# Kernel optimization log

Measured on AMD Instinct MI355X. Metric: run time of the kernel, lower is better.

Reference implementation:

```python
import jax, jax.numpy as jnp
import numpy as np

VOCAB = 32000
HID = 256
B = 16
S = 256


def setup_inputs() -> dict:
    key = jax.random.key(0)
    ks = jax.random.split(key, 8)
    old = jax.random.randint(ks[0], (B, S), 0, VOCAB)
    emb = jax.random.normal(ks[1], (VOCAB, HID), dtype=jnp.float32) * 0.05
    # PyTorch LSTM packs gates as [i, f, g, o] along dim 0 of weight matrices
    W_ih = jax.random.normal(ks[2], (4 * HID, HID), dtype=jnp.float32) * 0.05
    W_hh = jax.random.normal(ks[3], (4 * HID, HID), dtype=jnp.float32) * 0.05
    b_ih = jax.random.normal(ks[4], (4 * HID,), dtype=jnp.float32) * 0.05
    b_hh = jax.random.normal(ks[5], (4 * HID,), dtype=jnp.float32) * 0.05
    W_lin = jax.random.normal(ks[6], (VOCAB, HID), dtype=jnp.float32) * 0.05
    b_lin = jax.random.normal(ks[7], (VOCAB,), dtype=jnp.float32) * 0.05
    return {"old": old, "emb": emb, "W_ih": W_ih, "W_hh": W_hh,
            "b_ih": b_ih, "b_hh": b_hh, "W_lin": W_lin, "b_lin": b_lin}


def reference(old, emb, W_ih, W_hh, b_ih, b_hh, W_lin, b_lin):
    # Teacher forcing (teacher_ratio=0.5 is truthy in the original, so the
    # input at step l is always old[:, l-1]). ret[:, l] = logits after
    # consuming old[:, l-1]; final return is ret[:, 1:] -> [B, S-1, V].
    emb_eff = emb.at[0].set(0.0)          # padding_idx=0
    tokens = old[:, : S - 1]               # [B, T] with T = S-1
    x = emb_eff[tokens]                    # [B, T, H]
    x_t = jnp.swapaxes(x, 0, 1)            # [T, B, H] time-major for scan

    def step(carry, xt):
        h, c = carry
        gates = xt @ W_ih.T + b_ih + h @ W_hh.T + b_hh   # [B, 4H]
        i, f, g, o = jnp.split(gates, 4, axis=-1)
        c = jax.nn.sigmoid(f) * c + jax.nn.sigmoid(i) * jnp.tanh(g)
        h = jax.nn.sigmoid(o) * jnp.tanh(c)
        return (h, c), h

    h0 = jnp.zeros((B, HID), dtype=x.dtype)
    c0 = jnp.zeros((B, HID), dtype=x.dtype)
    _, hs = jax.lax.scan(step, (h0, c0), x_t)            # [T, B, H]
    logits = hs @ W_lin.T + b_lin                        # [T, B, V]
    return jnp.swapaxes(logits, 0, 1)                    # [B, T, V]
```

## Files before the change

### kernel.cpp

```cpp
#include <hip/hip_runtime.h>
#include <hip/hip_bf16.h>
#include <stdint.h>
#include <stddef.h>

#define VOCAB 32000
#define HID 256
#define BATCH 16
#define SEQ 256
#define TSTEPS 255
#define NGATES 1024
#define NWG 4
#define MROWS (TSTEPS*BATCH)

typedef __attribute__((ext_vector_type(8))) __bf16 bf16x8;
typedef __attribute__((ext_vector_type(8))) short short8;
typedef __attribute__((ext_vector_type(4))) float floatx4;

__device__ __forceinline__ float sigmoidf_(float x) {
    return 1.0f / (1.0f + __expf(-x));
}
__device__ __forceinline__ float tanhf_(float x) {
    return 2.0f / (1.0f + __expf(-2.0f * x)) - 1.0f;
}

__device__ __forceinline__ bf16x8 cvt8(const float* __restrict__ p) {
    const floatx4* q = (const floatx4*)p;
    floatx4 x = q[0], y = q[1];
    bf16x8 r;
    r[0] = (__bf16)x[0]; r[1] = (__bf16)x[1]; r[2] = (__bf16)x[2]; r[3] = (__bf16)x[3];
    r[4] = (__bf16)y[0]; r[5] = (__bf16)y[1]; r[6] = (__bf16)y[2]; r[7] = (__bf16)y[3];
    return r;
}

__global__ __launch_bounds__(256) void k_cvt(const float* __restrict__ src,
                                             __bf16* __restrict__ dst) {
    size_t i = ((size_t)blockIdx.x * 256 + threadIdx.x) * 8;
    bf16x8 r = cvt8(src + i);
    *(bf16x8*)(dst + i) = r;
}

__global__ __launch_bounds__(256) void k_xw(const int* __restrict__ old,
                                            const float* __restrict__ emb,
                                            const __bf16* __restrict__ wih,
                                            const float* __restrict__ b_ih,
                                            const float* __restrict__ b_hh,
                                            float* __restrict__ xw) {
    int t = blockIdx.x;
    int tid = threadIdx.x;
    int wave = tid >> 6, lane = tid & 63, quad = lane >> 4, l16 = lane & 15;

    int tok = old[l16 * SEQ + t];
    bf16x8 a[8];
#pragma unroll
    for (int kt = 0; kt < 8; kt++) {
        if (tok == 0) {
            bf16x8 z;
#pragma unroll
            for (int j = 0; j < 8; j++) z[j] = (__bf16)0.0f;
            a[kt] = z;
        } else {
            a[kt] = cvt8(emb + (size_t)tok * HID + kt * 32 + quad * 8);
        }
    }

    float* xwt = xw + (size_t)t * NGATES * BATCH;
    for (int nt = 0; nt < 16; nt++) {
        int n = wave * 256 + nt * 16 + l16;
        floatx4 acc = {0.0f, 0.0f, 0.0f, 0.0f};
#pragma unroll
        for (int kt = 0; kt < 8; kt++) {
            bf16x8 bf = *(const bf16x8*)(wih + (size_t)n * HID + kt * 32 + quad * 8);
            acc = __builtin_amdgcn_mfma_f32_16x16x32_bf16(a[kt], bf, acc, 0, 0, 0);
        }
        float bias = b_ih[n] + b_hh[n];
        acc[0] += bias; acc[1] += bias; acc[2] += bias; acc[3] += bias;
        *(floatx4*)(xwt + n * BATCH + quad * 4) = acc;
    }
}

__global__ __launch_bounds__(256) void k_scan(const float* __restrict__ W_hh,
                                              const float* __restrict__ xw,
                                              __bf16* __restrict__ hbuf,
                                              int* __restrict__ flags) {
    int wg = blockIdx.x;
    int tid = threadIdx.x;
    int wave = tid >> 6, lane = tid & 63, quad = lane >> 4, l16 = lane & 15;
    int j0 = wg * 64 + wave * 16;
    int jj = j0 + l16;

    bf16x8 wf[4][8];
#pragma unroll
    for (int g = 0; g < 4; g++) {
        const float* wrow = W_hh + (size_t)(g * HID + jj) * HID;
#pragma unroll
        for (int kt = 0; kt < 8; kt++)
            wf[g][kt] = cvt8(wrow + kt * 32 + quad * 8);
    }

    float cr0 = 0.0f, cr1 = 0.0f, cr2 = 0.0f, cr3 = 0.0f;

    for (int t = 0; t < TSTEPS; t++) {
        if (t > 0) {
            if (tid == 0) {
                while (__hip_atomic_load(flags + (t - 1), __ATOMIC_RELAXED,
                                         __HIP_MEMORY_SCOPE_AGENT) < NWG) {}
            }
            __syncthreads();
            __builtin_amdgcn_fence(__ATOMIC_ACQUIRE, "agent");
        }
        const __bf16* hs = hbuf + (size_t)t * (BATCH * HID) + l16 * HID;
        bf16x8 a[8];
#pragma unroll
        for (int kt = 0; kt < 8; kt++)
            a[kt] = *(const bf16x8*)(hs + kt * 32 + quad * 8);

        const float* xwt = xw + (size_t)t * NGATES * BATCH;
        floatx4 acc[4];
#pragma unroll
        for (int g = 0; g < 4; g++)
            acc[g] = *(const floatx4*)(xwt + (size_t)(g * HID + jj) * BATCH + quad * 4);

#pragma unroll
        for (int g = 0; g < 4; g++)
#pragma unroll
            for (int kt = 0; kt < 8; kt++)
                acc[g] = __builtin_amdgcn_mfma_f32_16x16x32_bf16(a[kt], wf[g][kt], acc[g], 0, 0, 0);

        __bf16* hout = hbuf + (size_t)(t + 1) * (BATCH * HID);
        float c[4] = {cr0, cr1, cr2, cr3};
#pragma unroll
        for (int r = 0; r < 4; r++) {
            float iv = sigmoidf_(acc[0][r]);
            float fv = sigmoidf_(acc[1][r]);
            float gv = tanhf_(acc[2][r]);
            float ov = sigmoidf_(acc[3][r]);
            float cn = fv * c[r] + iv * gv;
            float h = ov * tanhf_(cn);
            c[r] = cn;
            hout[(quad * 4 + r) * HID + jj] = (__bf16)h;
        }
        cr0 = c[0]; cr1 = c[1]; cr2 = c[2]; cr3 = c[3];

        __syncthreads();
        if (tid == 0) {
            __hip_atomic_fetch_add(flags + t, 1, __ATOMIC_RELEASE,
                                   __HIP_MEMORY_SCOPE_AGENT);
        }
    }
}

#define K3_MT 128
#define K3_NT 128
#define K3_KC 64
#define K3_LDR 72

__global__ __launch_bounds__(256) void k_proj(const __bf16* __restrict__ hbuf,
                                              const __bf16* __restrict__ wl,
                                              const float* __restrict__ b_lin,
                                              float* __restrict__ out) {
    __shared__ short lA[K3_MT * K3_LDR];
    __shared__ short lB[K3_NT * K3_LDR];

    int tid = threadIdx.x;
    int wave = tid >> 6, lane = tid & 63, quad = lane >> 4, l16 = lane & 15;
    int wm = wave >> 1, wn = wave & 1;
    int m0 = blockIdx.y * K3_MT;
    int n0 = blockIdx.x * K3_NT;

    floatx4 acc[4][4];
#pragma unroll
    for (int i = 0; i < 4; i++)
#pragma unroll
        for (int j = 0; j < 4; j++)
            acc[i][j] = (floatx4){0.0f, 0.0f, 0.0f, 0.0f};

    const __bf16* Abase = hbuf + (size_t)BATCH * HID;

    int srow = tid >> 1;
    int scol = (tid & 1) * 32;

    for (int kc = 0; kc < 4; kc++) {
        int kbase = kc * K3_KC;
        {
            int m = m0 + srow;
            const __bf16* src = Abase + (size_t)m * HID + kbase + scol;
#pragma unroll
            for (int i = 0; i < 4; i++) {
                short8 v = (short8)0;
                if (m < MROWS) v = *(const short8*)(src + i * 8);
                *(short8*)&lA[srow * K3_LDR + scol + i * 8] = v;
            }
        }
        {
            const __bf16* src = wl + (size_t)(n0 + srow) * HID + kbase + scol;
#pragma unroll
            for (int i = 0; i < 4; i++)
                *(short8*)&lB[srow * K3_LDR + scol + i * 8] = *(const short8*)(src + i * 8);
        }
        __syncthreads();
#pragma unroll
        for (int kt = 0; kt < 2; kt++) {
            int ko = kt * 32 + quad * 8;
            bf16x8 af[4], bf[4];
#pragma unroll
            for (int mt = 0; mt < 4; mt++)
                af[mt] = *(bf16x8*)&lA[(wm * 64 + mt * 16 + l16) * K3_LDR + ko];
#pragma unroll
            for (int nt = 0; nt < 4; nt++)
                bf[nt] = *(bf16x8*)&lB[(wn * 64 + nt * 16 + l16) * K3_LDR + ko];
#pragma unroll
            for (int mt = 0; mt < 4; mt++)
#pragma unroll
                for (int nt = 0; nt < 4; nt++)
                    acc[mt][nt] = __builtin_amdgcn_mfma_f32_16x16x32_bf16(
                        af[mt], bf[nt], acc[mt][nt], 0, 0, 0);
        }
        __syncthreads();
    }

#pragma unroll
    for (int nt = 0; nt < 4; nt++) {
        int n = n0 + wn * 64 + nt * 16 + l16;
        float bias = b_lin[n];
#pragma unroll
        for (int mt = 0; mt < 4; mt++) {
            int mbase = m0 + wm * 64 + mt * 16 + quad * 4;
#pragma unroll
            for (int r = 0; r < 4; r++) {
                int m = mbase + r;
                if (m < MROWS) {
                    int b = m & 15, t = m >> 4;
                    out[(size_t)b * TSTEPS * VOCAB + (size_t)t * VOCAB + n] =
                        acc[mt][nt][r] + bias;
                }
            }
        }
    }
}

extern "C" void kernel_launch(void* const* d_in, const int* in_sizes, int n_in,
                              void* d_out, int out_size, void* d_ws, size_t ws_size,
                              hipStream_t stream) {
    const int*   old   = (const int*)d_in[0];
    const float* emb   = (const float*)d_in[1];
    const float* W_ih  = (const float*)d_in[2];
    const float* W_hh  = (const float*)d_in[3];
    const float* b_ih  = (const float*)d_in[4];
    const float* b_hh  = (const float*)d_in[5];
    const float* W_lin = (const float*)d_in[6];
    const float* b_lin = (const float*)d_in[7];
    float* out = (float*)d_out;

    char* ws = (char*)d_ws;
    float*  xw    = (float*)ws;
    __bf16* wl    = (__bf16*)(ws + 16711680);
    __bf16* wih   = (__bf16*)(ws + 16711680 + 16384000);
    __bf16* hbuf  = (__bf16*)(ws + 16711680 + 16384000 + 524288);
    int*    flags = (int*)(ws + 16711680 + 16384000 + 524288 + 2097152);

    hipMemsetAsync(hbuf, 0, (size_t)BATCH * HID * sizeof(__bf16), stream);
    hipMemsetAsync(flags, 0, 256 * sizeof(int), stream);

    k_cvt<<<dim3(VOCAB * HID / 2048), dim3(256), 0, stream>>>(W_lin, wl);
    k_cvt<<<dim3(NGATES * HID / 2048), dim3(256), 0, stream>>>(W_ih, wih);
    k_xw<<<dim3(TSTEPS), dim3(256), 0, stream>>>(old, emb, wih, b_ih, b_hh, xw);
    k_scan<<<dim3(NWG), dim3(256), 0, stream>>>(W_hh, xw, hbuf, flags);
    k_proj<<<dim3(VOCAB / K3_NT, (MROWS + K3_MT - 1) / K3_MT), dim3(256), 0, stream>>>(
        hbuf, wl, b_lin, out);
}
```

Measured before the change: 1.642 ms.

## Replace flag barrier in LSTM scan with tagged per-element hidden-state polling

The recurrent scan no longer uses a per-step atomic counter, block-wide __syncthreads and an acquire fence. Each hidden value is now stored as a 32-bit word: the bf16 value plus a 16-bit step tag. Consumers poll with 64-bit relaxed atomic loads until every tag matches the expected step, then unpack the words into MFMA operands. The next step's xw gate preactivations are also prefetched into registers one step ahead. Tags depend only on the step index and the buffer is never cleared, so words left over from a previous launch with the same step tag could be accepted before the current launch writes them. That leaves a cross-call staleness risk.

After: 3.050 ms. +85.8%, slower.

```diff
diff --git a/kernel.cpp b/kernel.cpp
--- a/kernel.cpp
+++ b/kernel.cpp
@@ -30,6 +30,10 @@
     r[0] = (__bf16)x[0]; r[1] = (__bf16)x[1]; r[2] = (__bf16)x[2]; r[3] = (__bf16)x[3];
     r[4] = (__bf16)y[0]; r[5] = (__bf16)y[1]; r[6] = (__bf16)y[2]; r[7] = (__bf16)y[3];
     return r;
+}
+
+__device__ __forceinline__ uint32_t tag16(int t) {
+    return (uint32_t)((((t ^ 0xC3) & 0xFF) << 8) | ((t ^ 0x5A) & 0xFF));
 }
 
 __global__ __launch_bounds__(256) void k_cvt(const float* __restrict__ src,
@@ -78,10 +82,10 @@
     }
 }
 
-__global__ __launch_bounds__(256) void k_scan(const float* __restrict__ W_hh,
-                                              const float* __restrict__ xw,
-                                              __bf16* __restrict__ hbuf,
-                                              int* __restrict__ flags) {
+__global__ __launch_bounds__(256, 1) void k_scan(const float* __restrict__ W_hh,
+                                                 const float* __restrict__ xw,
+                                                 __bf16* __restrict__ hbuf,
+                                                 uint32_t* __restrict__ hpk) {
     int wg = blockIdx.x;
     int tid = threadIdx.x;
     int wave = tid >> 6, lane = tid & 63, quad = lane >> 4, l16 = lane & 15;
@@ -97,28 +101,68 @@
             wf[g][kt] = cvt8(wrow + kt * 32 + quad * 8);
     }
 
+    {
+        uint32_t z = tag16(0) << 16;
+#pragma unroll
+        for (int r = 0; r < 4; r++)
+            __hip_atomic_store(hpk + (quad * 4 + r) * HID + jj, z,
+                               __ATOMIC_RELAXED, __HIP_MEMORY_SCOPE_AGENT);
+    }
+
     float cr0 = 0.0f, cr1 = 0.0f, cr2 = 0.0f, cr3 = 0.0f;
 
+    floatx4 accN[4];
+#pragma unroll
+    for (int g = 0; g < 4; g++)
+        accN[g] = *(const floatx4*)(xw + (size_t)(g * HID + jj) * BATCH + quad * 4);
+
     for (int t = 0; t < TSTEPS; t++) {
-        if (t > 0) {
-            if (tid == 0) {
-                while (__hip_atomic_load(flags + (t - 1), __ATOMIC_RELAXED,
-                                         __HIP_MEMORY_SCOPE_AGENT) < NWG) {}
+        floatx4 acc[4];
+#pragma unroll
+        for (int g = 0; g < 4; g++) acc[g] = accN[g];
+        if (t + 1 < TSTEPS) {
+            const float* xwn = xw + (size_t)(t + 1) * NGATES * BATCH;
+#pragma unroll
+            for (int g = 0; g < 4; g++)
+                accN[g] = *(const floatx4*)(xwn + (size_t)(g * HID + jj) * BATCH + quad * 4);
+        }
+
+        const uint32_t* hp = hpk + (size_t)t * (BATCH * HID) + l16 * HID + quad * 8;
+        uint32_t texp = tag16(t);
+        unsigned long long wq[8][4];
+        uint32_t bad;
+        do {
+#pragma unroll
+            for (int kt = 0; kt < 8; kt++)
+#pragma unroll
+                for (int p = 0; p < 4; p++)
+                    wq[kt][p] = __hip_atomic_load(
+                        (const unsigned long long*)(hp + kt * 32 + p * 2),
+                        __ATOMIC_RELAXED, __HIP_MEMORY_SCOPE_AGENT);
+            bad = 0;
+#pragma unroll
+            for (int kt = 0; kt < 8; kt++)
+#pragma unroll
+                for (int p = 0; p < 4; p++) {
+                    uint32_t w0 = (uint32_t)wq[kt][p];
+                    uint32_t w1 = (uint32_t)(wq[kt][p] >> 32);
+                    bad |= (w0 >> 16) ^ texp;
+                    bad |= (w1 >> 16) ^ texp;
+                }
+        } while (bad);
+
+        bf16x8 a[8];
+#pragma unroll
+        for (int kt = 0; kt < 8; kt++) {
+            union { uint32_t u[4]; bf16x8 v; } cv;
+#pragma unroll
+            for (int p = 0; p < 4; p++) {
+                uint32_t w0 = (uint32_t)wq[kt][p];
+                uint32_t w1 = (uint32_t)(wq[kt][p] >> 32);
+                cv.u[p] = (w0 & 0xFFFFu) | (w1 << 16);
             }
-            __syncthreads();
-            __builtin_amdgcn_fence(__ATOMIC_ACQUIRE, "agent");
-        }
-        const __bf16* hs = hbuf + (size_t)t * (BATCH * HID) + l16 * HID;
-        bf16x8 a[8];
-#pragma unroll
-        for (int kt = 0; kt < 8; kt++)
-            a[kt] = *(const bf16x8*)(hs + kt * 32 + quad * 8);
-
-        const float* xwt = xw + (size_t)t * NGATES * BATCH;
-        floatx4 acc[4];
-#pragma unroll
-        for (int g = 0; g < 4; g++)
-            acc[g] = *(const floatx4*)(xwt + (size_t)(g * HID + jj) * BATCH + quad * 4);
+            a[kt] = cv.v;
+        }
 
 #pragma unroll
         for (int g = 0; g < 4; g++)
@@ -126,7 +170,9 @@
             for (int kt = 0; kt < 8; kt++)
                 acc[g] = __builtin_amdgcn_mfma_f32_16x16x32_bf16(a[kt], wf[g][kt], acc[g], 0, 0, 0);
 
-        __bf16* hout = hbuf + (size_t)(t + 1) * (BATCH * HID);
+        __bf16*   hout = hbuf + (size_t)(t + 1) * (BATCH * HID);
+        uint32_t* hpo  = hpk  + (size_t)(t + 1) * (BATCH * HID);
+        uint32_t  otag = tag16(t + 1) << 16;
         float c[4] = {cr0, cr1, cr2, cr3};
 #pragma unroll
         for (int r = 0; r < 4; r++) {
@@ -137,15 +183,14 @@
             float cn = fv * c[r] + iv * gv;
             float h = ov * tanhf_(cn);
             c[r] = cn;
-            hout[(quad * 4 + r) * HID + jj] = (__bf16)h;
+            __bf16 hb = (__bf16)h;
+            hout[(quad * 4 + r) * HID + jj] = hb;
+            union { __bf16 b; uint16_t u; } cvb; cvb.b = hb;
+            __hip_atomic_store(hpo + (quad * 4 + r) * HID + jj,
+                               otag | (uint32_t)cvb.u,
+                               __ATOMIC_RELAXED, __HIP_MEMORY_SCOPE_AGENT);
         }
         cr0 = c[0]; cr1 = c[1]; cr2 = c[2]; cr3 = c[3];
-
-        __syncthreads();
-        if (tid == 0) {
-            __hip_atomic_fetch_add(flags + t, 1, __ATOMIC_RELEASE,
-                                   __HIP_MEMORY_SCOPE_AGENT);
-        }
     }
 }
 
@@ -252,19 +297,16 @@
     float* out = (float*)d_out;
 
     char* ws = (char*)d_ws;
-    float*  xw    = (float*)ws;
-    __bf16* wl    = (__bf16*)(ws + 16711680);
-    __bf16* wih   = (__bf16*)(ws + 16711680 + 16384000);
-    __bf16* hbuf  = (__bf16*)(ws + 16711680 + 16384000 + 524288);
-    int*    flags = (int*)(ws + 16711680 + 16384000 + 524288 + 2097152);
-
-    hipMemsetAsync(hbuf, 0, (size_t)BATCH * HID * sizeof(__bf16), stream);
-    hipMemsetAsync(flags, 0, 256 * sizeof(int), stream);
+    float*    xw   = (float*)ws;
+    __bf16*   wl   = (__bf16*)(ws + 16711680);
+    __bf16*   wih  = (__bf16*)(ws + 16711680 + 16384000);
+    __bf16*   hbuf = (__bf16*)(ws + 16711680 + 16384000 + 524288);
+    uint32_t* hpk  = (uint32_t*)(ws + 16711680 + 16384000 + 524288 + 2097152);
 
     k_cvt<<<dim3(VOCAB * HID / 2048), dim3(256), 0, stream>>>(W_lin, wl);
     k_cvt<<<dim3(NGATES * HID / 2048), dim3(256), 0, stream>>>(W_ih, wih);
     k_xw<<<dim3(TSTEPS), dim3(256), 0, stream>>>(old, emb, wih, b_ih, b_hh, xw);
-    k_scan<<<dim3(NWG), dim3(256), 0, stream>>>(W_hh, xw, hbuf, flags);
+    k_scan<<<dim3(NWG), dim3(256), 0, stream>>>(W_hh, xw, hbuf, hpk);
     k_proj<<<dim3(VOCAB / K3_NT, (MROWS + K3_MT - 1) / K3_MT), dim3(256), 0, stream>>>(
         hbuf, wl, b_lin, out);
 }
```
